# Optimization experiments

Measured on AMD Instinct MI355X. Metric: run time of the kernel, lower is better.

The kernel has to match this reference:

```python
import jax, jax.numpy as jnp
import numpy as np

H = 16  # num_heads


def rope_cos_sin(S, d):
    # interleaved RoPE tables: cos = [cos0,cos0,cos1,cos1,...], sin likewise
    pos = jnp.arange(S, dtype=jnp.float32)[:, None]            # [S,1]
    ids = jnp.arange(d // 2, dtype=jnp.float32)
    theta = jnp.power(10000.0, -2.0 * ids / d)                  # [d/2]
    ang = pos * theta                                           # [S,d/2]
    cos = jnp.repeat(jnp.cos(ang), 2, axis=-1)                  # [S,d]
    sin = jnp.repeat(jnp.sin(ang), 2, axis=-1)                  # [S,d]
    return cos, sin


def apply_rope(x, cos, sin):
    # x: [B,H,S,d]; x2 = [-x1, x0, -x3, x2, ...]
    x2 = jnp.stack([-x[..., 1::2], x[..., ::2]], axis=-1).reshape(x.shape)
    return x * cos + x2 * sin


def setup_inputs() -> dict:
    key = jax.random.key(0)
    ks = jax.random.split(key, 9)
    B, S, D = 2, 2048, 1024
    sc = 1.0 / np.sqrt(D)
    return {
        "x": jax.random.normal(ks[0], (B, S, D), dtype=jnp.float32),
        "Wq": jax.random.normal(ks[1], (D, D), dtype=jnp.float32) * sc,
        "bq": jnp.zeros((D,), dtype=jnp.float32),
        "Wk": jax.random.normal(ks[2], (D, D), dtype=jnp.float32) * sc,
        "bk": jnp.zeros((D,), dtype=jnp.float32),
        "Wv": jax.random.normal(ks[3], (D, D), dtype=jnp.float32) * sc,
        "bv": jnp.zeros((D,), dtype=jnp.float32),
        "Wo": jax.random.normal(ks[4], (D, D), dtype=jnp.float32) * sc,
        "bo": jnp.zeros((D,), dtype=jnp.float32),
    }


def reference(x, Wq, bq, Wk, bk, Wv, bv, Wo, bo):
    B, S, D = x.shape
    dk = D // H
    scale = dk ** -0.5  # lsa=False -> fixed scale
    # QKV projections -> [B,H,S,dk]
    q = (x @ Wq + bq).reshape(B, S, H, dk).transpose(0, 2, 1, 3)
    k = (x @ Wk + bk).reshape(B, S, H, dk).transpose(0, 2, 1, 3)
    v = (x @ Wv + bv).reshape(B, S, H, dk).transpose(0, 2, 1, 3)
    cos, sin = rope_cos_sin(S, dk)
    q = apply_rope(q, cos, sin)
    k = apply_rope(k, cos, sin)
    attn_scores = jnp.einsum('bhqd,bhkd->bhqk', q, k) * scale
    attn_weights = jax.nn.softmax(attn_scores, axis=-1)  # dropout p=0
    out = jnp.einsum('bhqk,bhkd->bhqd', attn_weights, v)
    out = out.transpose(0, 2, 1, 3).reshape(B, S, D)
    out = out @ Wo + bo
    return out, attn_weights
```

## Files before the change

### kernel.cpp

```cpp
#include <hip/hip_runtime.h>

typedef __attribute__((ext_vector_type(4))) float f32x4;
typedef __attribute__((ext_vector_type(4))) int   i32x4;
typedef __attribute__((ext_vector_type(8))) short bf16x8;
typedef __attribute__((ext_vector_type(4))) short s16x4;

#define HD 16
#define SQ 2048
#define DM 1024
#define DK 64
#define QSCALE 0.18033688011112042f

__device__ __forceinline__ short f2bf(float f){
  union { float f; unsigned u; } c; c.f = f;
  unsigned r = (c.u + 0x7FFFu + ((c.u >> 16) & 1u)) >> 16;
  return (short)r;
}
__device__ __forceinline__ f32x4 mfma16(bf16x8 a, bf16x8 b, f32x4 c){
  return __builtin_amdgcn_mfma_f32_16x16x32_bf16(a, b, c, 0, 0, 0);
}
__device__ __forceinline__ void gload16(const void* g, void* l){
  __builtin_amdgcn_global_load_lds(
      (const __attribute__((address_space(1))) unsigned*)g,
      (__attribute__((address_space(3))) unsigned*)l, 16, 0, 0);
}

__global__ void k_prep(const float* __restrict__ x, short* __restrict__ xb,
    const float* __restrict__ W0, const float* __restrict__ W1,
    const float* __restrict__ W2, const float* __restrict__ W3,
    short* __restrict__ T0, short* __restrict__ T1,
    short* __restrict__ T2, short* __restrict__ T3,
    float2* __restrict__ rope)
{
  __shared__ float t[32][33];
  const int bid = blockIdx.x, tid = threadIdx.x;
  if (bid < 4096) {
    int i = (bid * 256 + tid) * 4;
    f32x4 v = *(const f32x4*)(x + i);
    s16x4 o;
    o[0] = f2bf(v[0]); o[1] = f2bf(v[1]); o[2] = f2bf(v[2]); o[3] = f2bf(v[3]);
    *(s16x4*)(xb + i) = o;
  } else if (bid < 8192) {
    int rem = bid - 4096;
    int z = rem >> 10, rxy = rem & 1023;
    int bx = rxy & 31, by = rxy >> 5;
    const float* W = (z == 0) ? W0 : (z == 1) ? W1 : (z == 2) ? W2 : W3;
    short* Wt = (z == 0) ? T0 : (z == 1) ? T1 : (z == 2) ? T2 : T3;
    int kx = bx * 32, nx = by * 32;
    int lx = tid & 31, ly = tid >> 5;
#pragma unroll
    for (int i2 = 0; i2 < 32; i2 += 8)
      t[ly + i2][lx] = W[(size_t)(kx + ly + i2) * DM + nx + lx];
    __syncthreads();
#pragma unroll
    for (int i2 = 0; i2 < 32; i2 += 8)
      Wt[(size_t)(nx + ly + i2) * DM + kx + lx] = f2bf(t[lx][ly + i2]);
  } else {
    int i = (bid - 8192) * 256 + tid;
    int s = i >> 5, d2 = i & 31;
    float theta = powf(10000.0f, -(float)d2 / 32.0f);
    float ang = (float)s * theta;
    rope[i] = make_float2(cosf(ang), sinf(ang));
  }
}

__global__ __launch_bounds__(256) void k_projqkv(const short* __restrict__ A,
    const short* __restrict__ Wqt, const short* __restrict__ Wkt, const short* __restrict__ Wvt,
    const float* __restrict__ bq, const float* __restrict__ bk, const float* __restrict__ bv,
    const float2* __restrict__ rope,
    short* __restrict__ Qo, short* __restrict__ Ko, short* __restrict__ Vo)
{
  __shared__ short As[128 * 64];
  __shared__ short Bs[128 * 64];
  const int mat = blockIdx.y >> 3;
  const int n0 = (blockIdx.y & 7) * 128;
  const short* Bt  = (mat == 0) ? Wqt : (mat == 1) ? Wkt : Wvt;
  const float* bias = (mat == 0) ? bq : (mat == 1) ? bk : bv;
  const int tid = threadIdx.x;
  const int lane = tid & 63, w = tid >> 6;
  const int wr = w >> 1, wc = w & 1;
  const int l15 = lane & 15, l4 = lane >> 4;
  const int m0 = blockIdx.x * 128;
  f32x4 acc[4][4] = {};

  for (int k0 = 0; k0 < DM; k0 += 64) {
#pragma unroll
    for (int i = 0; i < 4; ++i) {
      int c = w * 4 + i;
      int row = c * 8 + (lane >> 3);
      int so = (((lane & 7) * 16) ^ ((row & 7) << 4)) >> 1;
      gload16(A  + (size_t)(m0 + row) * DM + k0 + so, (char*)As + c * 1024);
      gload16(Bt + (size_t)(n0 + row) * DM + k0 + so, (char*)Bs + c * 1024);
    }
    __syncthreads();
#pragma unroll
    for (int kk = 0; kk < 64; kk += 32) {
      bf16x8 af[4], bfr[4];
#pragma unroll
      for (int mi = 0; mi < 4; ++mi) {
        int r = wr * 64 + mi * 16 + l15;
        af[mi] = *(const bf16x8*)((char*)As + ((r * 128 + kk * 2 + l4 * 16) ^ ((r & 7) << 4)));
      }
#pragma unroll
      for (int ni = 0; ni < 4; ++ni) {
        int r = wc * 64 + ni * 16 + l15;
        bfr[ni] = *(const bf16x8*)((char*)Bs + ((r * 128 + kk * 2 + l4 * 16) ^ ((r & 7) << 4)));
      }
#pragma unroll
      for (int mi = 0; mi < 4; ++mi)
#pragma unroll
        for (int ni = 0; ni < 4; ++ni)
          acc[mi][ni] = mfma16(af[mi], bfr[ni], acc[mi][ni]);
    }
    __syncthreads();
  }

#pragma unroll
  for (int mi = 0; mi < 4; ++mi) {
#pragma unroll
    for (int ni = 0; ni < 4; ++ni) {
      int n = n0 + wc * 64 + ni * 16 + l15;
      float bv2 = bias[n];
      if (mat == 2) {
        s16x4 pk;
        int mb = m0 + wr * 64 + mi * 16 + l4 * 4;
#pragma unroll
        for (int r2 = 0; r2 < 4; ++r2) pk[r2] = f2bf(acc[mi][ni][r2] + bv2);
        int b = mb >> 11, s = mb & 2047, h = n >> 6, d = n & 63;
        *(s16x4*)(Vo + ((size_t)((b * HD + h) * DK + d)) * SQ + s) = pk;
      } else {
        short* outp = (mat == 0) ? Qo : Ko;
        float sc = (mat == 0) ? QSCALE : 1.0f;
#pragma unroll
        for (int r2 = 0; r2 < 4; ++r2) {
          int m = m0 + wr * 64 + mi * 16 + l4 * 4 + r2;
          float v = acc[mi][ni][r2] + bv2;
          float pr = __shfl_xor(v, 1);
          int s = m & 2047, d = n & 63;
          float2 cs = rope[(s << 5) + (d >> 1)];
          v = (d & 1) ? (v * cs.x + pr * cs.y) : (v * cs.x - pr * cs.y);
          v *= sc;
          int b = m >> 11, h = n >> 6;
          outp[((size_t)((b * HD + h) * SQ + s)) * DK + d] = f2bf(v);
        }
      }
    }
  }
}

__global__ __launch_bounds__(256) void k_projO(const short* __restrict__ A, const short* __restrict__ Bt,
                                               const float* __restrict__ bias, float* __restrict__ out)
{
  __shared__ short As[64 * 64];
  __shared__ short Bs[128 * 64];
  const int tid = threadIdx.x;
  const int lane = tid & 63, w = tid >> 6;
  const int wr = w >> 1, wc = w & 1;
  const int l15 = lane & 15, l4 = lane >> 4;
  const int m0 = blockIdx.x * 64, n0 = blockIdx.y * 128;
  f32x4 acc[2][4] = {};

  for (int k0 = 0; k0 < DM; k0 += 64) {
#pragma unroll
    for (int i = 0; i < 2; ++i) {
      int c = w * 2 + i;
      int row = c * 8 + (lane >> 3);
      int so = (((lane & 7) * 16) ^ ((row & 7) << 4)) >> 1;
      gload16(A + (size_t)(m0 + row) * DM + k0 + so, (char*)As + c * 1024);
    }
#pragma unroll
    for (int i = 0; i < 4; ++i) {
      int c = w * 4 + i;
      int row = c * 8 + (lane >> 3);
      int so = (((lane & 7) * 16) ^ ((row & 7) << 4)) >> 1;
      gload16(Bt + (size_t)(n0 + row) * DM + k0 + so, (char*)Bs + c * 1024);
    }
    __syncthreads();
#pragma unroll
    for (int kk = 0; kk < 64; kk += 32) {
      bf16x8 af[2], bfr[4];
#pragma unroll
      for (int mi = 0; mi < 2; ++mi) {
        int r = wr * 32 + mi * 16 + l15;
        af[mi] = *(const bf16x8*)((char*)As + ((r * 128 + kk * 2 + l4 * 16) ^ ((r & 7) << 4)));
      }
#pragma unroll
      for (int ni = 0; ni < 4; ++ni) {
        int r = wc * 64 + ni * 16 + l15;
        bfr[ni] = *(const bf16x8*)((char*)Bs + ((r * 128 + kk * 2 + l4 * 16) ^ ((r & 7) << 4)));
      }
#pragma unroll
      for (int mi = 0; mi < 2; ++mi)
#pragma unroll
        for (int ni = 0; ni < 4; ++ni)
          acc[mi][ni] = mfma16(af[mi], bfr[ni], acc[mi][ni]);
    }
    __syncthreads();
  }

#pragma unroll
  for (int mi = 0; mi < 2; ++mi)
#pragma unroll
    for (int ni = 0; ni < 4; ++ni) {
      int n = n0 + wc * 64 + ni * 16 + l15;
      float bv2 = bias[n];
#pragma unroll
      for (int r2 = 0; r2 < 4; ++r2) {
        int m = m0 + wr * 32 + mi * 16 + l4 * 4 + r2;
        out[(size_t)m * DM + n] = acc[mi][ni][r2] + bv2;
      }
    }
}

__global__ __launch_bounds__(256, 4) void k_attn2(const short* __restrict__ Q, const short* __restrict__ K,
    const short* __restrict__ Vt, float* __restrict__ attn_out, short* __restrict__ ctx)
{
  __shared__ short KV4[4][64 * 64];
  __shared__ short Ps[64 * 64];
  const int idx = blockIdx.x;
  const int xcd = idx & 7, g = idx >> 3;
  const int bh = xcd * 4 + (g >> 5);
  const int qt = g & 31;
  const int tid = threadIdx.x, lane = tid & 63, w = tid >> 6;
  const int l15 = lane & 15, l4 = lane >> 4;
  const int qg = w >> 1, kg = w & 1;
  const short* Qg = Q + (size_t)(bh * SQ + qt * 64) * DK;
  const short* Kg = K + (size_t)bh * SQ * DK;
  const short* Vg = Vt + (size_t)bh * DK * SQ;
  char* KVb = (char*)KV4;

  const int c0 = w * 2, c1 = w * 2 + 1;
  const int row0 = c0 * 8 + (lane >> 3), row1 = c1 * 8 + (lane >> 3);
  const int so0 = (((lane & 7) * 16) ^ ((row0 & 7) << 4)) >> 1;
  const int so1 = (((lane & 7) * 16) ^ ((row1 & 7) << 4)) >> 1;

  bf16x8 q_b[2][2];
#pragma unroll
  for (int qs = 0; qs < 2; ++qs)
#pragma unroll
    for (int kx = 0; kx < 2; ++kx)
      q_b[qs][kx] = *(const bf16x8*)(Qg + (qg * 32 + qs * 16 + l15) * 64 + kx * 32 + l4 * 8);

  gload16(Kg + (size_t)row0 * 64 + so0, KVb + 0 * 8192 + c0 * 1024);
  gload16(Kg + (size_t)row1 * 64 + so1, KVb + 0 * 8192 + c1 * 1024);
  gload16(Kg + (size_t)(64 + row0) * 64 + so0, KVb + 1 * 8192 + c0 * 1024);
  gload16(Kg + (size_t)(64 + row1) * 64 + so1, KVb + 1 * 8192 + c1 * 1024);
  __syncthreads();
  float rs[2] = {0.0f, 0.0f};
  for (int i = 0; i < 16; ++i) {
    int cur = (i & 1) * 2;
    if (i < 15) {
      int nb = (i + 1) * 128, ns = cur ^ 2;
      gload16(Kg + (size_t)(nb + row0) * 64 + so0, KVb + ns * 8192 + c0 * 1024);
      gload16(Kg + (size_t)(nb + row1) * 64 + so1, KVb + ns * 8192 + c1 * 1024);
      gload16(Kg + (size_t)(nb + 64 + row0) * 64 + so0, KVb + (ns + 1) * 8192 + c0 * 1024);
      gload16(Kg + (size_t)(nb + 64 + row1) * 64 + so1, KVb + (ns + 1) * 8192 + c1 * 1024);
    }
#pragma unroll
    for (int sl = 0; sl < 2; ++sl) {
      const char* Kc = KVb + (cur + sl) * 8192;
      bf16x8 af[2][2];
#pragma unroll
      for (int ks = 0; ks < 2; ++ks)
#pragma unroll
        for (int kx = 0; kx < 2; ++kx) {
          int r = kg * 32 + ks * 16 + l15;
          af[ks][kx] = *(const bf16x8*)(Kc + ((r * 128 + kx * 64 + l4 * 16) ^ ((r & 7) << 4)));
        }
#pragma unroll
      for (int qs = 0; qs < 2; ++qs)
#pragma unroll
        for (int ks = 0; ks < 2; ++ks) {
          f32x4 p = {};
          p = mfma16(af[ks][0], q_b[qs][0], p);
          p = mfma16(af[ks][1], q_b[qs][1], p);
#pragma unroll
          for (int r2 = 0; r2 < 4; ++r2) rs[qs] += exp2f(p[r2]);
        }
    }
    __syncthreads();
  }
  float rv[2];
#pragma unroll
  for (int qs = 0; qs < 2; ++qs) {
    float v = rs[qs];
    v += __shfl_xor(v, 16);
    v += __shfl_xor(v, 32);
    rv[qs] = v;
  }
  {
    float* rst = (float*)Ps;
    if (lane < 16) {
#pragma unroll
      for (int qs = 0; qs < 2; ++qs)
        rst[(((qg * 2 + qs) * 16 + l15) * 2) + kg] = rv[qs];
    }
    __syncthreads();
#pragma unroll
    for (int qs = 0; qs < 2; ++qs)
      rv[qs] = 1.0f / (rv[qs] + rst[(((qg * 2 + qs) * 16 + l15) * 2) + (kg ^ 1)]);
  }
  const float rinv0 = rv[0], rinv1 = rv[1];

  f32x4 c[2][4] = {};
  float* attn_base = attn_out + ((size_t)(bh * SQ + qt * 64)) * SQ;

  gload16(Kg + (size_t)row0 * 64 + so0, KVb + 0 * 8192 + c0 * 1024);
  gload16(Kg + (size_t)row1 * 64 + so1, KVb + 0 * 8192 + c1 * 1024);
  gload16(Vg + (size_t)row0 * SQ + so0, KVb + 2 * 8192 + c0 * 1024);
  gload16(Vg + (size_t)row1 * SQ + so1, KVb + 2 * 8192 + c1 * 1024);
  __syncthreads();
  for (int t = 0; t < 32; ++t) {
    int cur = t & 1;
    if (t < 31) {
      gload16(Kg + (size_t)((t + 1) * 64 + row0) * 64 + so0, KVb + (cur ^ 1) * 8192 + c0 * 1024);
      gload16(Kg + (size_t)((t + 1) * 64 + row1) * 64 + so1, KVb + (cur ^ 1) * 8192 + c1 * 1024);
      gload16(Vg + (size_t)row0 * SQ + (t + 1) * 64 + so0, KVb + (2 + (cur ^ 1)) * 8192 + c0 * 1024);
      gload16(Vg + (size_t)row1 * SQ + (t + 1) * 64 + so1, KVb + (2 + (cur ^ 1)) * 8192 + c1 * 1024);
    }
    const char* Kc = KVb + cur * 8192;
    const char* Vc = KVb + (2 + cur) * 8192;
    bf16x8 af[2][2];
#pragma unroll
    for (int ks = 0; ks < 2; ++ks)
#pragma unroll
      for (int kx = 0; kx < 2; ++kx) {
        int r = kg * 32 + ks * 16 + l15;
        af[ks][kx] = *(const bf16x8*)(Kc + ((r * 128 + kx * 64 + l4 * 16) ^ ((r & 7) << 4)));
      }
#pragma unroll
    for (int qs = 0; qs < 2; ++qs) {
      const float rinv = qs ? rinv1 : rinv0;
#pragma unroll
      for (int ks = 0; ks < 2; ++ks) {
        f32x4 p = {};
        p = mfma16(af[ks][0], q_b[qs][0], p);
        p = mfma16(af[ks][1], q_b[qs][1], p);
        f32x4 wv;
        s16x4 pk;
#pragma unroll
        for (int r2 = 0; r2 < 4; ++r2) {
          wv[r2] = exp2f(p[r2]) * rinv;
          pk[r2] = f2bf(wv[r2]);
        }
        int qr = qg * 32 + qs * 16 + l15;
        __builtin_nontemporal_store(wv,
            (f32x4*)(attn_base + (size_t)qr * SQ + t * 64 + kg * 32 + ks * 16 + l4 * 4));
        *(s16x4*)((char*)Ps + ((qr * 128 + kg * 64 + ks * 32 + l4 * 8) ^ ((qr & 7) << 4))) = pk;
      }
    }
#pragma unroll
    for (int qs = 0; qs < 2; ++qs) {
      int qr = qg * 32 + qs * 16 + l15;
      bf16x8 ap = *(const bf16x8*)((char*)Ps + ((qr * 128 + kg * 64 + l4 * 16) ^ ((qr & 7) << 4)));
#pragma unroll
      for (int ds = 0; ds < 4; ++ds) {
        int r = ds * 16 + l15;
        bf16x8 bv = *(const bf16x8*)(Vc + ((r * 128 + kg * 64 + l4 * 16) ^ ((r & 7) << 4)));
        c[qs][ds] = mfma16(ap, bv, c[qs][ds]);
      }
    }
    __syncthreads();
  }
  float* red = (float*)KV4;
  if (kg == 1) {
#pragma unroll
    for (int qs = 0; qs < 2; ++qs)
#pragma unroll
      for (int ds = 0; ds < 4; ++ds)
#pragma unroll
        for (int r2 = 0; r2 < 4; ++r2)
          red[(qg * 32 + qs * 16 + l4 * 4 + r2) * 64 + ds * 16 + l15] = c[qs][ds][r2];
  }
  __syncthreads();
  if (kg == 0) {
    int b = bh >> 4, h = bh & 15;
#pragma unroll
    for (int qs = 0; qs < 2; ++qs)
#pragma unroll
      for (int ds = 0; ds < 4; ++ds)
#pragma unroll
        for (int r2 = 0; r2 < 4; ++r2) {
          int qr = qg * 32 + qs * 16 + l4 * 4 + r2;
          float v = c[qs][ds][r2] + red[qr * 64 + ds * 16 + l15];
          int s = qt * 64 + qr, d = ds * 16 + l15;
          ctx[((size_t)(b * SQ + s)) * DM + h * DK + d] = f2bf(v);
        }
  }
}

extern "C" void kernel_launch(void* const* d_in, const int* in_sizes, int n_in,
                              void* d_out, int out_size, void* d_ws, size_t ws_size,
                              hipStream_t stream)
{
  const float* x  = (const float*)d_in[0];
  const float* Wq = (const float*)d_in[1];
  const float* bq = (const float*)d_in[2];
  const float* Wk = (const float*)d_in[3];
  const float* bk = (const float*)d_in[4];
  const float* Wv = (const float*)d_in[5];
  const float* bv = (const float*)d_in[6];
  const float* Wo = (const float*)d_in[7];
  const float* bo = (const float*)d_in[8];

  char* p = (char*)d_ws;
  float2* rope = (float2*)p;  p += (size_t)SQ * 32 * sizeof(float2);
  short* xb  = (short*)p;     p += (size_t)4096 * DM * 2;
  short* Wqt = (short*)p;     p += (size_t)DM * DM * 2;
  short* Wkt = (short*)p;     p += (size_t)DM * DM * 2;
  short* Wvt = (short*)p;     p += (size_t)DM * DM * 2;
  short* Wot = (short*)p;     p += (size_t)DM * DM * 2;
  short* Qr  = (short*)p;     p += (size_t)2 * HD * SQ * DK * 2;
  short* Kr  = (short*)p;     p += (size_t)2 * HD * SQ * DK * 2;
  short* Vtr = (short*)p;     p += (size_t)2 * HD * SQ * DK * 2;
  short* ctx = (short*)p;     p += (size_t)4096 * DM * 2;

  k_prep<<<8448, 256, 0, stream>>>(x, xb, Wq, Wk, Wv, Wo, Wqt, Wkt, Wvt, Wot, rope);
  k_projqkv<<<dim3(32, 24), 256, 0, stream>>>(xb, Wqt, Wkt, Wvt, bq, bk, bv, rope, Qr, Kr, Vtr);
  float* attn = (float*)d_out + (size_t)2 * SQ * DM;
  k_attn2<<<1024, 256, 0, stream>>>(Qr, Kr, Vtr, attn, ctx);
  k_projO<<<dim3(64, 8), 256, 0, stream>>>(ctx, Wot, bo, (float*)d_out);
}
```

Before: 262.2 us.

## Load V fragments directly from global into registers, widen K tiles to 128

The second attention pass no longer stages V through LDS. Each lane loads its V^T MFMA operand fragments straight from global memory into registers, prefetching the next sub-tile's fragments one step ahead. The freed LDS slots let K be staged as 128-key double-buffered tiles, which halves the number of block barriers per pass. The cost is more register pressure and uncoalesced 16-byte global loads per lane, with latency that has to be hidden by the register prefetch.

```diff
diff --git a/kernel.cpp b/kernel.cpp
--- a/kernel.cpp
+++ b/kernel.cpp
@@ -212,6 +212,48 @@
     }
 }
 
+#define SUBTILE(Kc, KEY0, V0, V1, V2, V3)                                                  \
+  {                                                                                        \
+    bf16x8 af[2][2];                                                                       \
+    _Pragma("unroll")                                                                      \
+    for (int ks = 0; ks < 2; ++ks)                                                         \
+      _Pragma("unroll")                                                                    \
+      for (int kx = 0; kx < 2; ++kx) {                                                     \
+        int r = kg * 32 + ks * 16 + l15;                                                   \
+        af[ks][kx] = *(const bf16x8*)((Kc) + ((r * 128 + kx * 64 + l4 * 16) ^ ((r & 7) << 4))); \
+      }                                                                                    \
+    _Pragma("unroll")                                                                      \
+    for (int qs = 0; qs < 2; ++qs) {                                                       \
+      const float rinv = qs ? rinv1 : rinv0;                                               \
+      _Pragma("unroll")                                                                    \
+      for (int ks = 0; ks < 2; ++ks) {                                                     \
+        f32x4 p = {};                                                                      \
+        p = mfma16(af[ks][0], q_b[qs][0], p);                                              \
+        p = mfma16(af[ks][1], q_b[qs][1], p);                                              \
+        f32x4 wv;                                                                          \
+        s16x4 pk;                                                                          \
+        _Pragma("unroll")                                                                  \
+        for (int r2 = 0; r2 < 4; ++r2) {                                                   \
+          wv[r2] = exp2f(p[r2]) * rinv;                                                    \
+          pk[r2] = f2bf(wv[r2]);                                                           \
+        }                                                                                  \
+        int qr = qg * 32 + qs * 16 + l15;                                                  \
+        __builtin_nontemporal_store(wv,                                                    \
+            (f32x4*)(attn_base + (size_t)qr * SQ + (KEY0) + kg * 32 + ks * 16 + l4 * 4));  \
+        *(s16x4*)((char*)Ps + ((qr * 128 + kg * 64 + ks * 32 + l4 * 8) ^ ((qr & 7) << 4))) = pk; \
+      }                                                                                    \
+    }                                                                                      \
+    _Pragma("unroll")                                                                      \
+    for (int qs = 0; qs < 2; ++qs) {                                                       \
+      int qr = qg * 32 + qs * 16 + l15;                                                    \
+      bf16x8 ap = *(const bf16x8*)((char*)Ps + ((qr * 128 + kg * 64 + l4 * 16) ^ ((qr & 7) << 4))); \
+      c[qs][0] = mfma16(ap, (V0), c[qs][0]);                                               \
+      c[qs][1] = mfma16(ap, (V1), c[qs][1]);                                               \
+      c[qs][2] = mfma16(ap, (V2), c[qs][2]);                                               \
+      c[qs][3] = mfma16(ap, (V3), c[qs][3]);                                               \
+    }                                                                                      \
+  }
+
 __global__ __launch_bounds__(256, 4) void k_attn2(const short* __restrict__ Q, const short* __restrict__ K,
     const short* __restrict__ Vt, float* __restrict__ attn_out, short* __restrict__ ctx)
 {
@@ -234,6 +276,8 @@
   const int so0 = (((lane & 7) * 16) ^ ((row0 & 7) << 4)) >> 1;
   const int so1 = (((lane & 7) * 16) ^ ((row1 & 7) << 4)) >> 1;
 
+  const short* Vl = Vg + (size_t)l15 * SQ + kg * 32 + l4 * 8;
+
   bf16x8 q_b[2][2];
 #pragma unroll
   for (int qs = 0; qs < 2; ++qs)
@@ -307,58 +351,37 @@
 
   gload16(Kg + (size_t)row0 * 64 + so0, KVb + 0 * 8192 + c0 * 1024);
   gload16(Kg + (size_t)row1 * 64 + so1, KVb + 0 * 8192 + c1 * 1024);
-  gload16(Vg + (size_t)row0 * SQ + so0, KVb + 2 * 8192 + c0 * 1024);
-  gload16(Vg + (size_t)row1 * SQ + so1, KVb + 2 * 8192 + c1 * 1024);
+  gload16(Kg + (size_t)(64 + row0) * 64 + so0, KVb + 1 * 8192 + c0 * 1024);
+  gload16(Kg + (size_t)(64 + row1) * 64 + so1, KVb + 1 * 8192 + c1 * 1024);
+  bf16x8 vA0 = *(const bf16x8*)(Vl + 0 * SQ * 16);
+  bf16x8 vA1 = *(const bf16x8*)(Vl + 1 * SQ * 16);
+  bf16x8 vA2 = *(const bf16x8*)(Vl + 2 * SQ * 16);
+  bf16x8 vA3 = *(const bf16x8*)(Vl + 3 * SQ * 16);
   __syncthreads();
-  for (int t = 0; t < 32; ++t) {
-    int cur = t & 1;
-    if (t < 31) {
-      gload16(Kg + (size_t)((t + 1) * 64 + row0) * 64 + so0, KVb + (cur ^ 1) * 8192 + c0 * 1024);
-      gload16(Kg + (size_t)((t + 1) * 64 + row1) * 64 + so1, KVb + (cur ^ 1) * 8192 + c1 * 1024);
-      gload16(Vg + (size_t)row0 * SQ + (t + 1) * 64 + so0, KVb + (2 + (cur ^ 1)) * 8192 + c0 * 1024);
-      gload16(Vg + (size_t)row1 * SQ + (t + 1) * 64 + so1, KVb + (2 + (cur ^ 1)) * 8192 + c1 * 1024);
-    }
-    const char* Kc = KVb + cur * 8192;
-    const char* Vc = KVb + (2 + cur) * 8192;
-    bf16x8 af[2][2];
-#pragma unroll
-    for (int ks = 0; ks < 2; ++ks)
-#pragma unroll
-      for (int kx = 0; kx < 2; ++kx) {
-        int r = kg * 32 + ks * 16 + l15;
-        af[ks][kx] = *(const bf16x8*)(Kc + ((r * 128 + kx * 64 + l4 * 16) ^ ((r & 7) << 4)));
-      }
-#pragma unroll
-    for (int qs = 0; qs < 2; ++qs) {
-      const float rinv = qs ? rinv1 : rinv0;
-#pragma unroll
-      for (int ks = 0; ks < 2; ++ks) {
-        f32x4 p = {};
-        p = mfma16(af[ks][0], q_b[qs][0], p);
-        p = mfma16(af[ks][1], q_b[qs][1], p);
-        f32x4 wv;
-        s16x4 pk;
-#pragma unroll
-        for (int r2 = 0; r2 < 4; ++r2) {
-          wv[r2] = exp2f(p[r2]) * rinv;
-          pk[r2] = f2bf(wv[r2]);
-        }
-        int qr = qg * 32 + qs * 16 + l15;
-        __builtin_nontemporal_store(wv,
-            (f32x4*)(attn_base + (size_t)qr * SQ + t * 64 + kg * 32 + ks * 16 + l4 * 4));
-        *(s16x4*)((char*)Ps + ((qr * 128 + kg * 64 + ks * 32 + l4 * 8) ^ ((qr & 7) << 4))) = pk;
-      }
-    }
-#pragma unroll
-    for (int qs = 0; qs < 2; ++qs) {
-      int qr = qg * 32 + qs * 16 + l15;
-      bf16x8 ap = *(const bf16x8*)((char*)Ps + ((qr * 128 + kg * 64 + l4 * 16) ^ ((qr & 7) << 4)));
-#pragma unroll
-      for (int ds = 0; ds < 4; ++ds) {
-        int r = ds * 16 + l15;
-        bf16x8 bv = *(const bf16x8*)(Vc + ((r * 128 + kg * 64 + l4 * 16) ^ ((r & 7) << 4)));
-        c[qs][ds] = mfma16(ap, bv, c[qs][ds]);
-      }
+  for (int i = 0; i < 16; ++i) {
+    int cs = (i & 1) * 2;
+    if (i < 15) {
+      int nb = (i + 1) * 128, ns = cs ^ 2;
+      gload16(Kg + (size_t)(nb + row0) * 64 + so0, KVb + ns * 8192 + c0 * 1024);
+      gload16(Kg + (size_t)(nb + row1) * 64 + so1, KVb + ns * 8192 + c1 * 1024);
+      gload16(Kg + (size_t)(nb + 64 + row0) * 64 + so0, KVb + (ns + 1) * 8192 + c0 * 1024);
+      gload16(Kg + (size_t)(nb + 64 + row1) * 64 + so1, KVb + (ns + 1) * 8192 + c1 * 1024);
+    }
+    {
+      const short* Vb_ = Vl + i * 128 + 64;
+      bf16x8 vB0 = *(const bf16x8*)(Vb_ + 0 * SQ * 16);
+      bf16x8 vB1 = *(const bf16x8*)(Vb_ + 1 * SQ * 16);
+      bf16x8 vB2 = *(const bf16x8*)(Vb_ + 2 * SQ * 16);
+      bf16x8 vB3 = *(const bf16x8*)(Vb_ + 3 * SQ * 16);
+      SUBTILE(KVb + cs * 8192, i * 128, vA0, vA1, vA2, vA3)
+      if (i < 15) {
+        const short* Vn = Vl + (i + 1) * 128;
+        vA0 = *(const bf16x8*)(Vn + 0 * SQ * 16);
+        vA1 = *(const bf16x8*)(Vn + 1 * SQ * 16);
+        vA2 = *(const bf16x8*)(Vn + 2 * SQ * 16);
+        vA3 = *(const bf16x8*)(Vn + 3 * SQ * 16);
+      }
+      SUBTILE(KVb + (cs + 1) * 8192, i * 128 + 64, vB0, vB1, vB2, vB3)
     }
     __syncthreads();
   }
```

After: 267.3 us. About the same (+1.9%).

## Split attention into rowsum pass and smaller-tile output kernel with direct V loads

Applied to the files above, without the earlier changes.

The fused two-pass attention kernel is split into a separate row-sum kernel, which writes reciprocal softmax denominators to workspace, and an output kernel that reads them. The output kernel uses 32-row query tiles over 2048 blocks with a higher occupancy hint, and V is read directly from global memory instead of staged in LDS. This aims to raise parallelism and cut LDS use. In exchange it adds a launch and a workspace round trip, and the direct V loads are strided and partly redundant.

```diff
diff --git a/kernel.cpp b/kernel.cpp
--- a/kernel.cpp
+++ b/kernel.cpp
@@ -212,11 +212,11 @@
     }
 }
 
-__global__ __launch_bounds__(256, 4) void k_attn2(const short* __restrict__ Q, const short* __restrict__ K,
-    const short* __restrict__ Vt, float* __restrict__ attn_out, short* __restrict__ ctx)
-{
-  __shared__ short KV4[4][64 * 64];
-  __shared__ short Ps[64 * 64];
+__global__ __launch_bounds__(256, 4) void k_rowsum(const short* __restrict__ Q, const short* __restrict__ K,
+                                                   float* __restrict__ rinvg)
+{
+  __shared__ short K4[4][64 * 64];
+  __shared__ float rst[128];
   const int idx = blockIdx.x;
   const int xcd = idx & 7, g = idx >> 3;
   const int bh = xcd * 4 + (g >> 5);
@@ -226,8 +226,7 @@
   const int qg = w >> 1, kg = w & 1;
   const short* Qg = Q + (size_t)(bh * SQ + qt * 64) * DK;
   const short* Kg = K + (size_t)bh * SQ * DK;
-  const short* Vg = Vt + (size_t)bh * DK * SQ;
-  char* KVb = (char*)KV4;
+  char* KVb = (char*)K4;
 
   const int c0 = w * 2, c1 = w * 2 + 1;
   const int row0 = c0 * 8 + (lane >> 3), row1 = c1 * 8 + (lane >> 3);
@@ -288,38 +287,63 @@
     v += __shfl_xor(v, 32);
     rv[qs] = v;
   }
-  {
-    float* rst = (float*)Ps;
-    if (lane < 16) {
-#pragma unroll
-      for (int qs = 0; qs < 2; ++qs)
-        rst[(((qg * 2 + qs) * 16 + l15) * 2) + kg] = rv[qs];
-    }
-    __syncthreads();
+  if (lane < 16) {
 #pragma unroll
     for (int qs = 0; qs < 2; ++qs)
-      rv[qs] = 1.0f / (rv[qs] + rst[(((qg * 2 + qs) * 16 + l15) * 2) + (kg ^ 1)]);
-  }
-  const float rinv0 = rv[0], rinv1 = rv[1];
-
-  f32x4 c[2][4] = {};
-  float* attn_base = attn_out + ((size_t)(bh * SQ + qt * 64)) * SQ;
-
-  gload16(Kg + (size_t)row0 * 64 + so0, KVb + 0 * 8192 + c0 * 1024);
-  gload16(Kg + (size_t)row1 * 64 + so1, KVb + 0 * 8192 + c1 * 1024);
-  gload16(Vg + (size_t)row0 * SQ + so0, KVb + 2 * 8192 + c0 * 1024);
-  gload16(Vg + (size_t)row1 * SQ + so1, KVb + 2 * 8192 + c1 * 1024);
+      rst[(((qg * 2 + qs) * 16 + l15) * 2) + kg] = rv[qs];
+  }
+  __syncthreads();
+  if (lane < 16 && kg == 0) {
+#pragma unroll
+    for (int qs = 0; qs < 2; ++qs) {
+      float tot = rv[qs] + rst[(((qg * 2 + qs) * 16 + l15) * 2) + 1];
+      rinvg[bh * SQ + qt * 64 + qg * 32 + qs * 16 + l15] = 1.0f / tot;
+    }
+  }
+}
+
+__global__ __launch_bounds__(256, 6) void k_attn(const short* __restrict__ Q, const short* __restrict__ K,
+    const short* __restrict__ Vt, const float* __restrict__ rinvg,
+    float* __restrict__ attn_out, short* __restrict__ ctx)
+{
+  __shared__ short Kb[2][64 * 64];
+  __shared__ short Ps[32 * 64];
+  const int idx = blockIdx.x;
+  const int xcd = idx & 7, g = idx >> 3;
+  const int bh = xcd * 4 + (g >> 6);
+  const int qt = g & 63;
+  const int tid = threadIdx.x, lane = tid & 63, w = tid >> 6;
+  const int l15 = lane & 15, l4 = lane >> 4;
+  const int qg = w >> 1, kg = w & 1;
+  const short* Qg = Q + (size_t)(bh * SQ + qt * 32) * DK;
+  const short* Kg = K + (size_t)bh * SQ * DK;
+  const short* Vg = Vt + (size_t)bh * DK * SQ;
+
+  const int c0 = w * 2, c1 = w * 2 + 1;
+  const int row0 = c0 * 8 + (lane >> 3), row1 = c1 * 8 + (lane >> 3);
+  const int so0 = (((lane & 7) * 16) ^ ((row0 & 7) << 4)) >> 1;
+  const int so1 = (((lane & 7) * 16) ^ ((row1 & 7) << 4)) >> 1;
+
+  bf16x8 q_b[2];
+#pragma unroll
+  for (int kx = 0; kx < 2; ++kx)
+    q_b[kx] = *(const bf16x8*)(Qg + (qg * 16 + l15) * 64 + kx * 32 + l4 * 8);
+  const float rinv = rinvg[bh * SQ + qt * 32 + qg * 16 + l15];
+
+  f32x4 c[4] = {};
+  float* attn_base = attn_out + ((size_t)(bh * SQ + qt * 32)) * SQ;
+  const int qr = qg * 16 + l15;
+
+  gload16(Kg + (size_t)row0 * 64 + so0, (char*)Kb[0] + c0 * 1024);
+  gload16(Kg + (size_t)row1 * 64 + so1, (char*)Kb[0] + c1 * 1024);
   __syncthreads();
   for (int t = 0; t < 32; ++t) {
     int cur = t & 1;
     if (t < 31) {
-      gload16(Kg + (size_t)((t + 1) * 64 + row0) * 64 + so0, KVb + (cur ^ 1) * 8192 + c0 * 1024);
-      gload16(Kg + (size_t)((t + 1) * 64 + row1) * 64 + so1, KVb + (cur ^ 1) * 8192 + c1 * 1024);
-      gload16(Vg + (size_t)row0 * SQ + (t + 1) * 64 + so0, KVb + (2 + (cur ^ 1)) * 8192 + c0 * 1024);
-      gload16(Vg + (size_t)row1 * SQ + (t + 1) * 64 + so1, KVb + (2 + (cur ^ 1)) * 8192 + c1 * 1024);
-    }
-    const char* Kc = KVb + cur * 8192;
-    const char* Vc = KVb + (2 + cur) * 8192;
+      gload16(Kg + (size_t)((t + 1) * 64 + row0) * 64 + so0, (char*)Kb[cur ^ 1] + c0 * 1024);
+      gload16(Kg + (size_t)((t + 1) * 64 + row1) * 64 + so1, (char*)Kb[cur ^ 1] + c1 * 1024);
+    }
+    const char* Kc = (const char*)Kb[cur];
     bf16x8 af[2][2];
 #pragma unroll
     for (int ks = 0; ks < 2; ++ks)
@@ -329,63 +353,51 @@
         af[ks][kx] = *(const bf16x8*)(Kc + ((r * 128 + kx * 64 + l4 * 16) ^ ((r & 7) << 4)));
       }
 #pragma unroll
-    for (int qs = 0; qs < 2; ++qs) {
-      const float rinv = qs ? rinv1 : rinv0;
-#pragma unroll
-      for (int ks = 0; ks < 2; ++ks) {
-        f32x4 p = {};
-        p = mfma16(af[ks][0], q_b[qs][0], p);
-        p = mfma16(af[ks][1], q_b[qs][1], p);
-        f32x4 wv;
-        s16x4 pk;
-#pragma unroll
-        for (int r2 = 0; r2 < 4; ++r2) {
-          wv[r2] = exp2f(p[r2]) * rinv;
-          pk[r2] = f2bf(wv[r2]);
-        }
-        int qr = qg * 32 + qs * 16 + l15;
-        __builtin_nontemporal_store(wv,
-            (f32x4*)(attn_base + (size_t)qr * SQ + t * 64 + kg * 32 + ks * 16 + l4 * 4));
-        *(s16x4*)((char*)Ps + ((qr * 128 + kg * 64 + ks * 32 + l4 * 8) ^ ((qr & 7) << 4))) = pk;
-      }
-    }
-#pragma unroll
-    for (int qs = 0; qs < 2; ++qs) {
-      int qr = qg * 32 + qs * 16 + l15;
+    for (int ks = 0; ks < 2; ++ks) {
+      f32x4 p = {};
+      p = mfma16(af[ks][0], q_b[0], p);
+      p = mfma16(af[ks][1], q_b[1], p);
+      f32x4 wv;
+      s16x4 pk;
+#pragma unroll
+      for (int r2 = 0; r2 < 4; ++r2) {
+        wv[r2] = exp2f(p[r2]) * rinv;
+        pk[r2] = f2bf(wv[r2]);
+      }
+      __builtin_nontemporal_store(wv,
+          (f32x4*)(attn_base + (size_t)qr * SQ + t * 64 + kg * 32 + ks * 16 + l4 * 4));
+      *(s16x4*)((char*)Ps + ((qr * 128 + kg * 64 + ks * 32 + l4 * 8) ^ ((qr & 7) << 4))) = pk;
+    }
+    {
       bf16x8 ap = *(const bf16x8*)((char*)Ps + ((qr * 128 + kg * 64 + l4 * 16) ^ ((qr & 7) << 4)));
 #pragma unroll
       for (int ds = 0; ds < 4; ++ds) {
-        int r = ds * 16 + l15;
-        bf16x8 bv = *(const bf16x8*)(Vc + ((r * 128 + kg * 64 + l4 * 16) ^ ((r & 7) << 4)));
-        c[qs][ds] = mfma16(ap, bv, c[qs][ds]);
-      }
-    }
-    __syncthreads();
-  }
-  float* red = (float*)KV4;
+        bf16x8 bv = *(const bf16x8*)(Vg + (size_t)(ds * 16 + l15) * SQ + t * 64 + kg * 32 + l4 * 8);
+        c[ds] = mfma16(ap, bv, c[ds]);
+      }
+    }
+    __syncthreads();
+  }
+  float* red = (float*)Kb;
   if (kg == 1) {
 #pragma unroll
-    for (int qs = 0; qs < 2; ++qs)
-#pragma unroll
-      for (int ds = 0; ds < 4; ++ds)
-#pragma unroll
-        for (int r2 = 0; r2 < 4; ++r2)
-          red[(qg * 32 + qs * 16 + l4 * 4 + r2) * 64 + ds * 16 + l15] = c[qs][ds][r2];
+    for (int ds = 0; ds < 4; ++ds)
+#pragma unroll
+      for (int r2 = 0; r2 < 4; ++r2)
+        red[(qg * 16 + l4 * 4 + r2) * 64 + ds * 16 + l15] = c[ds][r2];
   }
   __syncthreads();
   if (kg == 0) {
     int b = bh >> 4, h = bh & 15;
 #pragma unroll
-    for (int qs = 0; qs < 2; ++qs)
-#pragma unroll
-      for (int ds = 0; ds < 4; ++ds)
-#pragma unroll
-        for (int r2 = 0; r2 < 4; ++r2) {
-          int qr = qg * 32 + qs * 16 + l4 * 4 + r2;
-          float v = c[qs][ds][r2] + red[qr * 64 + ds * 16 + l15];
-          int s = qt * 64 + qr, d = ds * 16 + l15;
-          ctx[((size_t)(b * SQ + s)) * DM + h * DK + d] = f2bf(v);
-        }
+    for (int ds = 0; ds < 4; ++ds)
+#pragma unroll
+      for (int r2 = 0; r2 < 4; ++r2) {
+        int qr2 = qg * 16 + l4 * 4 + r2;
+        float v = c[ds][r2] + red[qr2 * 64 + ds * 16 + l15];
+        int s = qt * 32 + qr2, d = ds * 16 + l15;
+        ctx[((size_t)(b * SQ + s)) * DM + h * DK + d] = f2bf(v);
+      }
   }
 }
 
@@ -413,11 +425,13 @@
   short* Qr  = (short*)p;     p += (size_t)2 * HD * SQ * DK * 2;
   short* Kr  = (short*)p;     p += (size_t)2 * HD * SQ * DK * 2;
   short* Vtr = (short*)p;     p += (size_t)2 * HD * SQ * DK * 2;
+  float* rinvg = (float*)p;   p += (size_t)2 * HD * SQ * 4;
   short* ctx = (short*)p;     p += (size_t)4096 * DM * 2;
 
   k_prep<<<8448, 256, 0, stream>>>(x, xb, Wq, Wk, Wv, Wo, Wqt, Wkt, Wvt, Wot, rope);
   k_projqkv<<<dim3(32, 24), 256, 0, stream>>>(xb, Wqt, Wkt, Wvt, bq, bk, bv, rope, Qr, Kr, Vtr);
+  k_rowsum<<<1024, 256, 0, stream>>>(Qr, Kr, rinvg);
   float* attn = (float*)d_out + (size_t)2 * SQ * DM;
-  k_attn2<<<1024, 256, 0, stream>>>(Qr, Kr, Vtr, attn, ctx);
+  k_attn<<<2048, 256, 0, stream>>>(Qr, Kr, Vtr, rinvg, attn, ctx);
   k_projO<<<dim3(64, 8), 256, 0, stream>>>(ctx, Wot, bo, (float*)d_out);
 }
```

New measurement: 276.4 us. 5.4% more time.
